# Optimization experiments

Hardware: AMD Instinct MI355X
Metric: run time of the kernel (lower is better)

## Reference

```python
import jax, jax.numpy as jnp
import numpy as np

KS = 3        # kernel_size
DIL = 2       # dilation
HEAD_DIM = 32


def _unfold(x, ks, dil):
    """torch nn.Unfold(ks, dilation=dil, padding=dil*(ks-1)//2, stride=1).
    x: [B, C, H, W] -> [B, C, ks*ks, H, W] (channel-major patch order, matching torch)."""
    B, C, H, W = x.shape
    pad = dil * (ks - 1) // 2
    xp = jnp.pad(x, ((0, 0), (0, 0), (pad, pad), (pad, pad)))
    pats = [xp[:, :, i * dil:i * dil + H, j * dil:j * dil + W]
            for i in range(ks) for j in range(ks)]
    return jnp.stack(pats, axis=2)


def setup_inputs() -> dict:
    key = jax.random.key(0)
    k1, k2, k3 = jax.random.split(key, 3)
    shape = (16, 128, 64, 64)  # [B, d, H, W]
    return {
        "q": jax.random.normal(k1, shape, dtype=jnp.float32),
        "k": jax.random.normal(k2, shape, dtype=jnp.float32),
        "v": jax.random.normal(k3, shape, dtype=jnp.float32),
    }


def reference(q, k, v):
    B, d, H, W = q.shape
    heads = d // HEAD_DIM
    scale = HEAD_DIM ** (-0.5)
    KK = KS * KS
    # q: [B, heads, head_dim, H*W]
    qr = q.reshape(B, heads, HEAD_DIM, H * W)
    # unfolded k/v: [B, heads, head_dim, KK, H*W]
    ku = _unfold(k, KS, DIL).reshape(B, heads, HEAD_DIM, KK, H * W)
    vu = _unfold(v, KS, DIL).reshape(B, heads, HEAD_DIM, KK, H * W)
    # per-pixel small attention over KK local dilated keys
    attn = jnp.einsum('bhdn,bhdkn->bhnk', qr, ku) * scale  # [B,heads,HW,KK]
    attn = jax.nn.softmax(attn, axis=-1)  # attn_drop = 0 -> identity
    out = jnp.einsum('bhnk,bhdkn->bnhd', attn, vu)  # [B,HW,heads,head_dim]
    return out.reshape(B, H, W, d)
```

## Files before the change

kernel.cpp:

```cpp
#include <hip/hip_runtime.h>

namespace {
constexpr float SCALE = 0.17677669529663687f;
constexpr int CHP = 194;

__global__ __launch_bounds__(256, 2) void dilate_attn(
    const float* __restrict__ q, const float* __restrict__ k,
    const float* __restrict__ v, float* __restrict__ out) {
  __shared__ float kbuf[32 * CHP];
  __shared__ float vbuf[32 * CHP];

  const int tid = threadIdx.x;
  const int cg  = tid & 7;
  const int pp  = tid >> 3;

  const int blk   = blockIdx.x;
  const int s     = blk >> 3;
  const int combo = ((blk & 7) << 3) | (s >> 6);
  const int h     = s & 63;
  const int b     = combo >> 2;
  const int head  = combo & 3;

  const size_t cb = ((size_t)b * 128 + head * 32) * 4096;
  const float* kp = k + cb;
  const float* vp = v + cb;

  int rows[3]; float rowm[3];
  #pragma unroll
  for (int r = 0; r < 3; ++r) {
    const int ry = h + 2 * (r - 1);
    const bool ok = (unsigned)ry < 64u;
    rows[r] = (ok ? ry : h) * 64;
    rowm[r] = ok ? 1.0f : 0.0f;
  }

  const int px0 = pp << 1;
  float2 q2[4];
  #pragma unroll
  for (int ci = 0; ci < 4; ++ci)
    q2[ci] = *(const float2*)(q + cb + (cg * 4 + ci) * 4096 + h * 64 + px0);

  #pragma unroll
  for (int t = 0; t < 6; ++t) {
    const int l4  = t * 256 + tid;
    const int ch  = l4 / 48;
    const int rem = l4 - ch * 48;
    const int r   = rem >> 4;
    const int p4  = (rem & 15) << 2;
    const int go  = ch * 4096 + rows[r] + p4;
    const float4 k4 = *(const float4*)(kp + go);
    const float4 v4 = *(const float4*)(vp + go);
    const int wo = ch * CHP + r * 64 + p4;
    ((float2*)(kbuf + wo))[0] = make_float2(k4.x, k4.y);
    ((float2*)(kbuf + wo))[1] = make_float2(k4.z, k4.w);
    ((float2*)(vbuf + wo))[0] = make_float2(v4.x, v4.y);
    ((float2*)(vbuf + wo))[1] = make_float2(v4.z, v4.w);
  }

  __syncthreads();

  const int   txL = (pp == 0)  ? 0  : px0 - 2;
  const int   txC = px0;
  const int   txR = (pp == 31) ? 62 : px0 + 2;
  const float mL  = (pp == 0)  ? 0.0f : 1.0f;
  const float mR  = (pp == 31) ? 0.0f : 1.0f;

  float l0[9], l1[9];
  #pragma unroll
  for (int t = 0; t < 9; ++t) { l0[t] = 0.0f; l1[t] = 0.0f; }

  #pragma unroll
  for (int r = 0; r < 3; ++r) {
    #pragma unroll
    for (int ci = 0; ci < 4; ++ci) {
      const float* kc = kbuf + (cg * 4 + ci) * CHP + r * 64;
      const float2 kL = *(const float2*)(kc + txL);
      const float2 kC = *(const float2*)(kc + txC);
      const float2 kR = *(const float2*)(kc + txR);
      const float2 qq = q2[ci];
      l0[r*3+0] = fmaf(qq.x, kL.x, l0[r*3+0]);
      l1[r*3+0] = fmaf(qq.y, kL.y, l1[r*3+0]);
      l0[r*3+1] = fmaf(qq.x, kC.x, l0[r*3+1]);
      l1[r*3+1] = fmaf(qq.y, kC.y, l1[r*3+1]);
      l0[r*3+2] = fmaf(qq.x, kR.x, l0[r*3+2]);
      l1[r*3+2] = fmaf(qq.y, kR.y, l1[r*3+2]);
    }
  }

  #pragma unroll
  for (int m = 1; m <= 4; m <<= 1) {
    #pragma unroll
    for (int t = 0; t < 9; ++t) {
      l0[t] += __shfl_xor(l0[t], m, 64);
      l1[t] += __shfl_xor(l1[t], m, 64);
    }
  }

  float msk[9];
  #pragma unroll
  for (int r = 0; r < 3; ++r) {
    msk[r*3+0] = rowm[r] * mL;
    msk[r*3+1] = rowm[r];
    msk[r*3+2] = rowm[r] * mR;
  }
  float mx0 = -1e30f, mx1 = -1e30f;
  #pragma unroll
  for (int t = 0; t < 9; ++t) {
    l0[t] *= msk[t]; l1[t] *= msk[t];
    mx0 = fmaxf(mx0, l0[t]); mx1 = fmaxf(mx1, l1[t]);
  }
  float s0 = 0.0f, s1 = 0.0f;
  #pragma unroll
  for (int t = 0; t < 9; ++t) {
    l0[t] = __expf((l0[t] - mx0) * SCALE);
    l1[t] = __expf((l1[t] - mx1) * SCALE);
    s0 += l0[t]; s1 += l1[t];
  }
  const float r0 = 1.0f / s0, r1 = 1.0f / s1;
  #pragma unroll
  for (int t = 0; t < 9; ++t) {
    l0[t] *= r0 * msk[t];
    l1[t] *= r1 * msk[t];
  }

  float o0[4] = {0, 0, 0, 0}, o1[4] = {0, 0, 0, 0};
  #pragma unroll
  for (int r = 0; r < 3; ++r) {
    #pragma unroll
    for (int ci = 0; ci < 4; ++ci) {
      const float* vc = vbuf + (cg * 4 + ci) * CHP + r * 64;
      const float2 vL = *(const float2*)(vc + txL);
      const float2 vC = *(const float2*)(vc + txC);
      const float2 vR = *(const float2*)(vc + txR);
      o0[ci] = fmaf(l0[r*3+0], vL.x, o0[ci]);
      o0[ci] = fmaf(l0[r*3+1], vC.x, o0[ci]);
      o0[ci] = fmaf(l0[r*3+2], vR.x, o0[ci]);
      o1[ci] = fmaf(l1[r*3+0], vL.y, o1[ci]);
      o1[ci] = fmaf(l1[r*3+1], vC.y, o1[ci]);
      o1[ci] = fmaf(l1[r*3+2], vR.y, o1[ci]);
    }
  }

  float* ob = out + ((size_t)(b * 64 + h) * 64 + px0) * 128 + head * 32 + cg * 4;
  *(float4*)(ob)       = make_float4(o0[0], o0[1], o0[2], o0[3]);
  *(float4*)(ob + 128) = make_float4(o1[0], o1[1], o1[2], o1[3]);
}
}

extern "C" void kernel_launch(void* const* d_in, const int* in_sizes, int n_in,
                              void* d_out, int out_size, void* d_ws, size_t ws_size,
                              hipStream_t stream) {
  const float* q = (const float*)d_in[0];
  const float* k = (const float*)d_in[1];
  const float* v = (const float*)d_in[2];
  float* o = (float*)d_out;
  dilate_attn<<<dim3(4096), dim3(256), 0, stream>>>(q, k, v, o);
}
```

Before: 148.3 us.

## Drop LDS staging and read K/V neighbors directly from global memory

Removes the shared-memory K/V tile and the block barrier, so each thread loads its dilated neighbor K and V values straight from global memory, relying on the L1/L2 caches for reuse. With no LDS in use, the launch bound is raised to allow more resident blocks. The softmax scale is folded into q at load time. In exchange, each value is fetched about three times per row from cache, with scattered float2 loads, instead of once per block with coalesced float4 loads.

```diff
diff --git a/kernel.cpp b/kernel.cpp
--- a/kernel.cpp
+++ b/kernel.cpp
@@ -2,14 +2,10 @@
 
 namespace {
 constexpr float SCALE = 0.17677669529663687f;
-constexpr int CHP = 194;
 
-__global__ __launch_bounds__(256, 2) void dilate_attn(
+__global__ __launch_bounds__(256, 4) void dilate_attn(
     const float* __restrict__ q, const float* __restrict__ k,
     const float* __restrict__ v, float* __restrict__ out) {
-  __shared__ float kbuf[32 * CHP];
-  __shared__ float vbuf[32 * CHP];
-
   const int tid = threadIdx.x;
   const int cg  = tid & 7;
   const int pp  = tid >> 3;
@@ -22,8 +18,6 @@
   const int head  = combo & 3;
 
   const size_t cb = ((size_t)b * 128 + head * 32) * 4096;
-  const float* kp = k + cb;
-  const float* vp = v + cb;
 
   int rows[3]; float rowm[3];
   #pragma unroll
@@ -37,33 +31,20 @@
   const int px0 = pp << 1;
   float2 q2[4];
   #pragma unroll
-  for (int ci = 0; ci < 4; ++ci)
+  for (int ci = 0; ci < 4; ++ci) {
     q2[ci] = *(const float2*)(q + cb + (cg * 4 + ci) * 4096 + h * 64 + px0);
-
-  #pragma unroll
-  for (int t = 0; t < 6; ++t) {
-    const int l4  = t * 256 + tid;
-    const int ch  = l4 / 48;
-    const int rem = l4 - ch * 48;
-    const int r   = rem >> 4;
-    const int p4  = (rem & 15) << 2;
-    const int go  = ch * 4096 + rows[r] + p4;
-    const float4 k4 = *(const float4*)(kp + go);
-    const float4 v4 = *(const float4*)(vp + go);
-    const int wo = ch * CHP + r * 64 + p4;
-    ((float2*)(kbuf + wo))[0] = make_float2(k4.x, k4.y);
-    ((float2*)(kbuf + wo))[1] = make_float2(k4.z, k4.w);
-    ((float2*)(vbuf + wo))[0] = make_float2(v4.x, v4.y);
-    ((float2*)(vbuf + wo))[1] = make_float2(v4.z, v4.w);
+    q2[ci].x *= SCALE;
+    q2[ci].y *= SCALE;
   }
-
-  __syncthreads();
 
   const int   txL = (pp == 0)  ? 0  : px0 - 2;
   const int   txC = px0;
   const int   txR = (pp == 31) ? 62 : px0 + 2;
   const float mL  = (pp == 0)  ? 0.0f : 1.0f;
   const float mR  = (pp == 31) ? 0.0f : 1.0f;
+
+  const float* kp = k + cb + (size_t)(cg * 4) * 4096;
+  const float* vp = v + cb + (size_t)(cg * 4) * 4096;
 
   float l0[9], l1[9];
   #pragma unroll
@@ -73,7 +54,7 @@
   for (int r = 0; r < 3; ++r) {
     #pragma unroll
     for (int ci = 0; ci < 4; ++ci) {
-      const float* kc = kbuf + (cg * 4 + ci) * CHP + r * 64;
+      const float* kc = kp + ci * 4096 + rows[r];
       const float2 kL = *(const float2*)(kc + txL);
       const float2 kC = *(const float2*)(kc + txC);
       const float2 kR = *(const float2*)(kc + txR);
@@ -112,8 +93,8 @@
   float s0 = 0.0f, s1 = 0.0f;
   #pragma unroll
   for (int t = 0; t < 9; ++t) {
-    l0[t] = __expf((l0[t] - mx0) * SCALE);
-    l1[t] = __expf((l1[t] - mx1) * SCALE);
+    l0[t] = __expf(l0[t] - mx0);
+    l1[t] = __expf(l1[t] - mx1);
     s0 += l0[t]; s1 += l1[t];
   }
   const float r0 = 1.0f / s0, r1 = 1.0f / s1;
@@ -128,7 +109,7 @@
   for (int r = 0; r < 3; ++r) {
     #pragma unroll
     for (int ci = 0; ci < 4; ++ci) {
-      const float* vc = vbuf + (cg * 4 + ci) * CHP + r * 64;
+      const float* vc = vp + ci * 4096 + rows[r];
       const float2 vL = *(const float2*)(vc + txL);
       const float2 vC = *(const float2*)(vc + txC);
       const float2 vR = *(const float2*)(vc + txR);
```

Result: slower. 285.9 us (+92.8%).

## Stage K/V tiles with direct global-to-LDS loads and a rotated LDS layout

Applied to the files above, without the earlier changes.

Replaces the register-staged float4 loads and split float2 LDS stores with `__builtin_amdgcn_global_load_lds` 16-byte transfers straight into shared memory. The K/V row stride drops from a padded 194 to an unpadded 192, so bank conflicts are avoided by rotating each channel's pixel positions instead; the reads apply the matching per-channel rotation. The softmax scale is also folded into q once, removing a multiply per logit. This aims to cut VGPR traffic and instruction count in the load phase, but depends on lane-contiguous LDS addressing and adds modulo index arithmetic on the read side.

```diff
diff --git a/kernel.cpp b/kernel.cpp
--- a/kernel.cpp
+++ b/kernel.cpp
@@ -2,7 +2,10 @@
 
 namespace {
 constexpr float SCALE = 0.17677669529663687f;
-constexpr int CHP = 194;
+constexpr int CHP = 192;
+
+typedef const __attribute__((address_space(1))) void gbl_v;
+typedef __attribute__((address_space(3))) void lds_v;
 
 __global__ __launch_bounds__(256, 2) void dilate_attn(
     const float* __restrict__ q, const float* __restrict__ k,
@@ -37,8 +40,11 @@
   const int px0 = pp << 1;
   float2 q2[4];
   #pragma unroll
-  for (int ci = 0; ci < 4; ++ci)
+  for (int ci = 0; ci < 4; ++ci) {
     q2[ci] = *(const float2*)(q + cb + (cg * 4 + ci) * 4096 + h * 64 + px0);
+    q2[ci].x *= SCALE;
+    q2[ci].y *= SCALE;
+  }
 
   #pragma unroll
   for (int t = 0; t < 6; ++t) {
@@ -46,15 +52,12 @@
     const int ch  = l4 / 48;
     const int rem = l4 - ch * 48;
     const int r   = rem >> 4;
-    const int p4  = (rem & 15) << 2;
-    const int go  = ch * 4096 + rows[r] + p4;
-    const float4 k4 = *(const float4*)(kp + go);
-    const float4 v4 = *(const float4*)(vp + go);
-    const int wo = ch * CHP + r * 64 + p4;
-    ((float2*)(kbuf + wo))[0] = make_float2(k4.x, k4.y);
-    ((float2*)(kbuf + wo))[1] = make_float2(k4.z, k4.w);
-    ((float2*)(vbuf + wo))[0] = make_float2(v4.x, v4.y);
-    ((float2*)(vbuf + wo))[1] = make_float2(v4.z, v4.w);
+    const int q4  = rem & 15;
+    const int pxs = ((q4 - (ch & 7)) & 15) << 2;
+    const int go  = ch * 4096 + rows[r] + pxs;
+    const int lo  = l4 << 2;
+    __builtin_amdgcn_global_load_lds((gbl_v*)(kp + go), (lds_v*)(kbuf + lo), 16, 0, 0);
+    __builtin_amdgcn_global_load_lds((gbl_v*)(vp + go), (lds_v*)(vbuf + lo), 16, 0, 0);
   }
 
   __syncthreads();
@@ -65,6 +68,15 @@
   const float mL  = (pp == 0)  ? 0.0f : 1.0f;
   const float mR  = (pp == 31) ? 0.0f : 1.0f;
 
+  int tL[4], tC[4], tR[4];
+  #pragma unroll
+  for (int ci = 0; ci < 4; ++ci) {
+    const int rot = ((cg & 1) << 4) | (ci << 2);
+    tL[ci] = (txL + rot) & 63;
+    tC[ci] = (txC + rot) & 63;
+    tR[ci] = (txR + rot) & 63;
+  }
+
   float l0[9], l1[9];
   #pragma unroll
   for (int t = 0; t < 9; ++t) { l0[t] = 0.0f; l1[t] = 0.0f; }
@@ -74,9 +86,9 @@
     #pragma unroll
     for (int ci = 0; ci < 4; ++ci) {
       const float* kc = kbuf + (cg * 4 + ci) * CHP + r * 64;
-      const float2 kL = *(const float2*)(kc + txL);
-      const float2 kC = *(const float2*)(kc + txC);
-      const float2 kR = *(const float2*)(kc + txR);
+      const float2 kL = *(const float2*)(kc + tL[ci]);
+      const float2 kC = *(const float2*)(kc + tC[ci]);
+      const float2 kR = *(const float2*)(kc + tR[ci]);
       const float2 qq = q2[ci];
       l0[r*3+0] = fmaf(qq.x, kL.x, l0[r*3+0]);
       l1[r*3+0] = fmaf(qq.y, kL.y, l1[r*3+0]);
@@ -112,8 +124,8 @@
   float s0 = 0.0f, s1 = 0.0f;
   #pragma unroll
   for (int t = 0; t < 9; ++t) {
-    l0[t] = __expf((l0[t] - mx0) * SCALE);
-    l1[t] = __expf((l1[t] - mx1) * SCALE);
+    l0[t] = __expf(l0[t] - mx0);
+    l1[t] = __expf(l1[t] - mx1);
     s0 += l0[t]; s1 += l1[t];
   }
   const float r0 = 1.0f / s0, r1 = 1.0f / s1;
@@ -129,9 +141,9 @@
     #pragma unroll
     for (int ci = 0; ci < 4; ++ci) {
       const float* vc = vbuf + (cg * 4 + ci) * CHP + r * 64;
-      const float2 vL = *(const float2*)(vc + txL);
-      const float2 vC = *(const float2*)(vc + txC);
-      const float2 vR = *(const float2*)(vc + txR);
+      const float2 vL = *(const float2*)(vc + tL[ci]);
+      const float2 vC = *(const float2*)(vc + tC[ci]);
+      const float2 vR = *(const float2*)(vc + tR[ci]);
       o0[ci] = fmaf(l0[r*3+0], vL.x, o0[ci]);
       o0[ci] = fmaf(l0[r*3+1], vC.x, o0[ci]);
       o0[ci] = fmaf(l0[r*3+2], vR.x, o0[ci]);
```

Result: slower. 151.5 us (+2.2%).
